# Kernel optimization log

Hardware: AMD Instinct MI355X
Metric: run time of the kernel (lower is better)

The kernel has to match this reference:

```python
import jax, jax.numpy as jnp
import numpy as np

N, C, K, B, G = 32768, 128, 16, 4, 8
SCALE, BASE = 2.0, 10000.0

def _bn(x, gamma, beta, eps=1e-5):
    # torch BatchNorm1d (training): stats over all axes except channel (last)
    axes = tuple(range(x.ndim - 1))
    mean = x.mean(axes)
    var = x.var(axes)
    return (x - mean) / jnp.sqrt(var + eps) * gamma + beta

def _cayley_rope(x, coord, S_param):
    c = x.shape[-1]
    S = jnp.triu(S_param, 1)
    S = S - S.T
    I = jnp.eye(c, dtype=x.dtype)
    P = jnp.linalg.solve(I + S, I - S)  # (I+S)^-1 (I-S)
    xr = x @ P.T
    dpa = c // 3 // 2 * 2          # dim per axis (even)
    dr = dpa * 3                   # rotated dims
    inv_freq = 1.0 / (BASE ** (jnp.arange(0, dpa, 2, dtype=jnp.float32) / dpa))
    cs = coord * SCALE
    def rot(f, c1):
        ang = c1[:, None] * inv_freq[None, :]
        s, co = jnp.sin(ang), jnp.cos(ang)
        fr, fi = jnp.split(f, 2, axis=-1)
        return jnp.concatenate([fr * co - fi * s, fr * s + fi * co], -1)
    parts = [rot(xr[:, i * dpa:(i + 1) * dpa], cs[:, i]) for i in range(3)]
    out = jnp.concatenate(parts + [xr[:, dr:]], -1)
    return out @ P

def setup_inputs() -> dict:
    key = jax.random.key(0)
    ks = jax.random.split(key, 24)
    w = lambda k, i, o, s=0.02: jax.random.normal(k, (i, o), jnp.float32) * s
    inp = {
        'feat': jax.random.normal(ks[0], (N, C), jnp.float32),
        'coord': jax.random.uniform(ks[1], (N, 3), jnp.float32) * 10.0,
        'reference_index': jax.random.randint(ks[2], (N, K), 0, N),
        'offset': jnp.arange(1, B + 1, dtype=jnp.int32) * (N // B),
        'Wq': w(ks[3], C, C), 'bq': jnp.zeros((C,)),
        'gq': jnp.ones((C,)), 'bnq': jnp.zeros((C,)),
        'Wk': w(ks[4], C, C), 'bk': jnp.zeros((C,)),
        'gk': jnp.ones((C,)), 'bnk': jnp.zeros((C,)),
        'Wv': w(ks[5], C, C), 'bv': jnp.zeros((C,)),
        'S_param': jax.random.normal(ks[6], (C, C), jnp.float32) * 0.01,
        'Ww1': w(ks[7], C, G), 'bw1': jnp.zeros((G,)),
        'gw': jnp.ones((G,)), 'bnw': jnp.zeros((G,)),
        'Ww2': w(ks[8], G, G), 'bw2': jnp.zeros((G,)),
        'Wg1': w(ks[9], 2 * C, C), 'bg1': jnp.zeros((C,)),
        'gg': jnp.ones((C,)), 'bng': jnp.zeros((C,)),
        'Wg2': w(ks[10], C, G, 0.001), 'bg2': jnp.full((G,), 3.0),
    }
    return inp

def reference(feat, coord, reference_index, offset, Wq, bq, gq, bnq, Wk, bk, gk, bnk,
              Wv, bv, S_param, Ww1, bw1, gw, bnw, Ww2, bw2, Wg1, bg1, gg, bng, Wg2, bg2):
    q_raw = jax.nn.relu(_bn(feat @ Wq + bq, gq, bnq))
    k_raw = jax.nn.relu(_bn(feat @ Wk + bk, gk, bnk))
    value = feat @ Wv + bv
    q = _cayley_rope(q_raw, coord, S_param)
    k = _cayley_rope(k_raw, coord, S_param)
    kg = k[reference_index]            # [N,K,C] gather
    vg = value[reference_index]        # [N,K,C]
    rel = kg - q[:, None, :]
    geom = jax.nn.relu(_bn(rel @ Ww1 + bw1, gw, bnw)) @ Ww2 + bw2  # [N,K,G]
    seg = jnp.searchsorted(offset, jnp.arange(N), side='right')
    gmax = jax.ops.segment_max(q_raw, seg, num_segments=B)
    gate_in = jnp.concatenate([q_raw, gmax[seg]], -1)              # [N,2C]
    gate = jax.nn.sigmoid(jax.nn.relu(_bn(gate_in @ Wg1 + bg1, gg, bng)) @ Wg2 + bg2)  # [N,G]
    refined = geom * (1.0 + gate[:, None, :])
    attn = jax.nn.softmax(refined, axis=1)
    mask = jnp.sign(reference_index + 1).astype(attn.dtype)
    attn = attn * mask[:, :, None]
    vg4 = vg.reshape(N, K, G, C // G)
    out = jnp.einsum('nkgi,nkg->ngi', vg4, attn).reshape(N, C)
    return out
```

## Files before the change

kernel.cpp:

```cpp
#include <hip/hip_runtime.h>
#include <math.h>

#define N_PTS 32768
#define C_DIM 128
#define K_NB  16
#define G_DIM 8

#define OF_PT     0
#define OF_PW     16384
#define OF_STATQ  17408
#define OF_STATK  17664
#define OF_STATG1 17920
#define OF_STATH  18176
#define OF_UMAXP  18192
#define OF_UMAXN  18704
#define OF_WQT    20480
#define OF_WKT    28672
#define OF_WVT    36864
#define OF_WG1T   45056
#define OF_PTMIT  53248
#define OF_QW     61440
#define OF_KW     323584
#define OF_GATE   585728
#define OF_BIG0   1048576
#define OF_BIG1   5242880
#define OF_BIG2   9437184
#define OF_BIG3   13631488

typedef short bf16x8 __attribute__((ext_vector_type(8)));
typedef float f32x4  __attribute__((ext_vector_type(4)));

__device__ __forceinline__ unsigned f2bf(float f) {
  unsigned u = __float_as_uint(f);
  return (u + 0x7fffu + ((u >> 16) & 1u)) >> 16;
}
__device__ __forceinline__ unsigned fenc(float f) {
  unsigned b = __float_as_uint(f);
  return (b & 0x80000000u) ? ~b : (b | 0x80000000u);
}
__device__ __forceinline__ float fdec(unsigned u) {
  unsigned b = (u & 0x80000000u) ? (u & 0x7fffffffu) : ~u;
  return __uint_as_float(b);
}
__device__ __forceinline__ bf16x8 pack_bf8(float4 a, float4 b) {
  bf16x8 r;
  r[0] = (short)f2bf(a.x); r[1] = (short)f2bf(a.y);
  r[2] = (short)f2bf(a.z); r[3] = (short)f2bf(a.w);
  r[4] = (short)f2bf(b.x); r[5] = (short)f2bf(b.y);
  r[6] = (short)f2bf(b.z); r[7] = (short)f2bf(b.w);
  return r;
}

struct MMJob {
  const float* A; const float* B; float* D;
  float s, a, b, c;
  int asymA, asymB;
};

__device__ __forceinline__ float fetch_asym(const float* M, int r, int c) {
  return (c > r) ? M[r*128 + c] : ((c < r) ? -M[c*128 + r] : 0.f);
}

__device__ __forceinline__ void mm_body(const MMJob& jb, int t, int tid)
{
  __shared__ float As[32][132];
  __shared__ float Bs[128][36];
  int tr = (t >> 2) * 32, tc = (t & 3) * 32;
  #pragma unroll
  for (int it = 0; it < 4; ++it) {
    int q = tid + it*256; int r = q >> 5, cq = q & 31;
    if (jb.asymA) {
      #pragma unroll
      for (int i = 0; i < 4; ++i) As[r][cq*4 + i] = fetch_asym(jb.A, tr + r, cq*4 + i);
    } else {
      *(float4*)&As[r][cq*4] = ((const float4*)jb.A)[(tr + r)*32 + cq];
    }
  }
  #pragma unroll
  for (int it = 0; it < 4; ++it) {
    int q = tid + it*256; int r = q >> 3, cq = q & 7;
    if (jb.asymB) {
      #pragma unroll
      for (int i = 0; i < 4; ++i) Bs[r][cq*4 + i] = fetch_asym(jb.B, r, tc + cq*4 + i);
    } else {
      *(float4*)&Bs[r][cq*4] = ((const float4*)jb.B)[r*32 + (tc >> 2) + cq];
    }
  }
  __syncthreads();
  int tx = tid & 15, ty = tid >> 4;
  int r0 = ty*2, c0 = tx*2;
  float acc[2][2] = {{0.f,0.f},{0.f,0.f}};
  #pragma unroll 8
  for (int k = 0; k < 128; ++k) {
    float a0 = As[r0][k], a1 = As[r0+1][k];
    float b0 = Bs[k][c0], b1 = Bs[k][c0+1];
    acc[0][0] = fmaf(a0, b0, acc[0][0]);
    acc[0][1] = fmaf(a0, b1, acc[0][1]);
    acc[1][0] = fmaf(a1, b0, acc[1][0]);
    acc[1][1] = fmaf(a1, b1, acc[1][1]);
  }
  #pragma unroll
  for (int dr = 0; dr < 2; ++dr) {
    #pragma unroll
    for (int dc = 0; dc < 2; ++dc) {
      int R = tr + r0 + dr, Cc = tc + c0 + dc;
      float v = jb.s * acc[dr][dc];
      if (jb.a != 0.f) {
        float av = jb.asymA ? fetch_asym(jb.A, R, Cc) : jb.A[R*128 + Cc];
        v = fmaf(jb.a, av, v);
      }
      if (jb.b != 0.f) {
        float bv = jb.asymB ? fetch_asym(jb.B, R, Cc) : jb.B[R*128 + Cc];
        v = fmaf(jb.b, bv, v);
      }
      if (R == Cc) v += jb.c;
      jb.D[R*128 + Cc] = v;
    }
  }
}

__global__ __launch_bounds__(256) void mm128(MMJob j0, MMJob j1)
{
  int bx = blockIdx.x;
  mm_body((bx < 16) ? j0 : j1, bx & 15, threadIdx.x);
}

__global__ __launch_bounds__(256) void chain1(const float* __restrict__ Sp, float* __restrict__ T1,
    const float* __restrict__ Wq, const float* __restrict__ Wk,
    const float* __restrict__ Wv, const float* __restrict__ Wg1,
    short* __restrict__ WqT, short* __restrict__ WkT,
    short* __restrict__ WvT, short* __restrict__ Wg1T,
    float* __restrict__ statz)
{
  int bx = blockIdx.x, tid = threadIdx.x;
  if (bx < 16) {
    MMJob j{Sp, Sp, T1, 1.f, 0.f, 0.f, 0.f, 1, 1};
    mm_body(j, bx, tid);
  } else if (bx == 16) {
    #pragma unroll
    for (int it = 0; it < 8; ++it) {
      int idx = it*256 + tid;
      if (idx < 1808) statz[idx] = 0.f;
    }
  } else {
    int idx = bx - 17, widx = idx >> 2, qr = idx & 3;
    const float* src = (widx == 0) ? Wq : (widx == 1) ? Wk : (widx == 2) ? Wv : Wg1;
    short* dst = (widx == 0) ? WqT : (widx == 1) ? WkT : (widx == 2) ? WvT : Wg1T;
    const float4* s4 = (const float4*)src;
    #pragma unroll
    for (int it = 0; it < 4; ++it) {
      int q = it*256 + tid; int k = qr*32 + (q >> 5), n4 = q & 31;
      float4 v = s4[k*32 + n4];
      dst[(n4*4+0)*128 + k] = (short)f2bf(v.x);
      dst[(n4*4+1)*128 + k] = (short)f2bf(v.y);
      dst[(n4*4+2)*128 + k] = (short)f2bf(v.z);
      dst[(n4*4+3)*128 + k] = (short)f2bf(v.w);
    }
  }
}

__global__ __launch_bounds__(1024) void pwprep(const float* __restrict__ PT,
                                               const float* __restrict__ Ww1,
                                               float* __restrict__ PW,
                                               short* __restrict__ PTmIT)
{
  __shared__ float pts[128*128];
  int tid = threadIdx.x, bx = blockIdx.x;
  if (bx == 0) {
    #pragma unroll
    for (int it = 0; it < 16; ++it) pts[tid + it*1024] = PT[tid + it*1024];
    __syncthreads();
    int i = tid & 127, g = tid >> 7;
    float acc = 0.f;
    #pragma unroll 8
    for (int j = 0; j < 128; ++j) acc = fmaf(pts[j*128 + i], Ww1[j*8 + g], acc);
    PW[i*8 + g] = acc;
  } else {
    int qr = bx - 1;
    #pragma unroll
    for (int it = 0; it < 4; ++it) {
      int q = it*1024 + tid;
      int k = qr*32 + (q >> 7), n = q & 127;
      float v = PT[k*128 + n] - ((k == n) ? 1.f : 0.f);
      PTmIT[n*128 + k] = (short)f2bf(v);
    }
  }
}

template<int MODE>
__device__ __forceinline__ void qkv_pass(const short* __restrict__ WT,
    const float* __restrict__ bias, float* __restrict__ Out,
    const bf16x8* af, int row0, int w, int l15, int quad, int lane,
    float* ssum, float* ssq, unsigned* ump, unsigned* umn)
{
  #pragma unroll
  for (int nt = 0; nt < 8; ++nt) {
    f32x4 ac = {0.f, 0.f, 0.f, 0.f};
    #pragma unroll
    for (int ks = 0; ks < 4; ++ks) {
      bf16x8 bf = *(const bf16x8*)&WT[(nt*16 + l15)*128 + ks*32 + quad*8];
      ac = __builtin_amdgcn_mfma_f32_16x16x32_bf16(af[ks], bf, ac, 0, 0, 0);
    }
    int col = nt*16 + l15;
    float bb = bias[col];
    float s = 0.f, s2 = 0.f, mx = -1e30f, mn = 1e30f;
    #pragma unroll
    for (int r = 0; r < 4; ++r) {
      float v = ac[r] + bb;
      int row = row0 + w*16 + quad*4 + r;
      Out[(long)row*128 + col] = v;
      if (MODE < 2) { s += v; s2 = fmaf(v, v, s2); }
      if (MODE == 0) { mx = fmaxf(mx, v); mn = fminf(mn, v); }
    }
    if (MODE < 2) {
      s += __shfl_xor(s, 16); s += __shfl_xor(s, 32);
      s2 += __shfl_xor(s2, 16); s2 += __shfl_xor(s2, 32);
      if (MODE == 0) {
        mx = fmaxf(mx, __shfl_xor(mx, 16)); mx = fmaxf(mx, __shfl_xor(mx, 32));
        mn = fminf(mn, __shfl_xor(mn, 16)); mn = fminf(mn, __shfl_xor(mn, 32));
      }
      if (lane < 16) {
        atomicAdd(&ssum[col], s); atomicAdd(&ssq[col], s2);
        if (MODE == 0) { atomicMax(&ump[col], fenc(mx)); atomicMax(&umn[col], fenc(-mn)); }
      }
    }
  }
}

__global__ __launch_bounds__(256) void qkv_mfma(const float* __restrict__ feat,
    const short* __restrict__ WqT, const short* __restrict__ WkT, const short* __restrict__ WvT,
    const float* __restrict__ bq, const float* __restrict__ bk, const float* __restrict__ bv,
    float* __restrict__ Aq, float* __restrict__ Bk, float* __restrict__ Vv,
    float* __restrict__ statq, float* __restrict__ statk,
    unsigned* __restrict__ umaxp, unsigned* __restrict__ umaxn)
{
  __shared__ float ssum[2][128], ssq[2][128];
  __shared__ unsigned ump[128], umn[128];
  int tid = threadIdx.x, row0 = blockIdx.x * 64, seg = row0 >> 13;
  if (tid < 128) {
    ssum[0][tid] = 0.f; ssum[1][tid] = 0.f;
    ssq[0][tid] = 0.f;  ssq[1][tid] = 0.f;
    ump[tid] = 0u; umn[tid] = 0u;
  }
  __syncthreads();
  int lane = tid & 63, w = tid >> 6, l15 = lane & 15, quad = lane >> 4;
  const float4* f4 = (const float4*)feat;
  bf16x8 af[4];
  #pragma unroll
  for (int ks = 0; ks < 4; ++ks) {
    long base = (long)(row0 + w*16 + l15)*32 + ks*8 + quad*2;
    float4 a0 = f4[base], a1 = f4[base + 1];
    af[ks] = pack_bf8(a0, a1);
  }
  qkv_pass<0>(WqT, bq, Aq, af, row0, w, l15, quad, lane, ssum[0], ssq[0], ump, umn);
  qkv_pass<1>(WkT, bk, Bk, af, row0, w, l15, quad, lane, ssum[1], ssq[1], ump, umn);
  qkv_pass<2>(WvT, bv, Vv, af, row0, w, l15, quad, lane, nullptr, nullptr, nullptr, nullptr);
  __syncthreads();
  if (tid < 128) {
    atomicAdd(&statq[tid], ssum[0][tid]); atomicAdd(&statq[128 + tid], ssq[0][tid]);
    atomicAdd(&statk[tid], ssum[1][tid]); atomicAdd(&statk[128 + tid], ssq[1][tid]);
    atomicMax(&umaxp[seg*128 + tid], ump[tid]);
    atomicMax(&umaxn[seg*128 + tid], umn[tid]);
  }
}

__global__ __launch_bounds__(256) void rqkw(
    const float* __restrict__ Aq, const float* __restrict__ Bk,
    const short* __restrict__ PTmIT, const short* __restrict__ Wg1T,
    const float* __restrict__ coord,
    const float* __restrict__ statq, const float* __restrict__ statk,
    const float* __restrict__ gq, const float* __restrict__ bnq,
    const float* __restrict__ gk, const float* __restrict__ bnk,
    const unsigned* __restrict__ umaxp, const unsigned* __restrict__ umaxn,
    const float* __restrict__ Wg1, const float* __restrict__ bg1,
    const float* __restrict__ PW, const float* __restrict__ bw1,
    float* __restrict__ qw, float* __restrict__ kw,
    float* __restrict__ g1, float* __restrict__ statg1)
{
  __shared__ float xsq[32*132], xsk[32*132];
  __shared__ float pws[128*8];
  __shared__ float caq[128], cbq[128], cak[128], cbk[128];
  __shared__ float gml[128], gsg[128];
  __shared__ float ssum[128], ssq[128];
  int tid = threadIdx.x;
  int row0 = blockIdx.x * 32, seg = row0 >> 13;
  const float invn = 1.f / 32768.f;
  if (tid < 128) {
    float m = statq[tid]*invn, vv = fmaf(-m, m, statq[128 + tid]*invn);
    float a = rsqrtf(vv + 1e-5f) * gq[tid];
    float b = fmaf(-m, a, bnq[tid]);
    caq[tid] = a; cbq[tid] = b;
    float mx = fdec(umaxp[seg*128 + tid]);
    float mn = -fdec(umaxn[seg*128 + tid]);
    gml[tid] = fmaxf(0.f, fmaxf(fmaf(a, mx, b), fmaf(a, mn, b)));
    m = statk[tid]*invn; vv = fmaf(-m, m, statk[128 + tid]*invn);
    a = rsqrtf(vv + 1e-5f) * gk[tid];
    cak[tid] = a; cbk[tid] = fmaf(-m, a, bnk[tid]);
    ssum[tid] = 0.f; ssq[tid] = 0.f;
  }
  #pragma unroll
  for (int it = 0; it < 4; ++it) { int idx = tid + it*256; pws[idx] = PW[idx]; }
  __syncthreads();
  if (tid < 128) {
    float acc = bg1[tid];
    #pragma unroll 8
    for (int j = 0; j < 128; ++j) acc = fmaf(gml[j], Wg1[(128 + j)*128 + tid], acc);
    gsg[tid] = acc;
  }
  int lane = tid & 63, w = tid >> 6, l15 = lane & 15, quad = lane >> 4;
  bool isq = (w < 2);
  const float* src = isq ? Aq : Bk;
  const float* ca = isq ? caq : cak;
  const float* cb = isq ? cbq : cbk;
  int rw = (w & 1) * 16;
  const float4* s4 = (const float4*)src;
  bf16x8 af[4];
  #pragma unroll
  for (int ks = 0; ks < 4; ++ks) {
    long base = (long)(row0 + rw + l15)*32 + ks*8 + quad*2;
    float4 a0 = s4[base], a1 = s4[base + 1];
    int c0 = ks*32 + quad*8;
    float4 r0, r1;
    r0.x = fmaxf(0.f, fmaf(ca[c0+0], a0.x, cb[c0+0]));
    r0.y = fmaxf(0.f, fmaf(ca[c0+1], a0.y, cb[c0+1]));
    r0.z = fmaxf(0.f, fmaf(ca[c0+2], a0.z, cb[c0+2]));
    r0.w = fmaxf(0.f, fmaf(ca[c0+3], a0.w, cb[c0+3]));
    r1.x = fmaxf(0.f, fmaf(ca[c0+4], a1.x, cb[c0+4]));
    r1.y = fmaxf(0.f, fmaf(ca[c0+5], a1.y, cb[c0+5]));
    r1.z = fmaxf(0.f, fmaf(ca[c0+6], a1.z, cb[c0+6]));
    r1.w = fmaxf(0.f, fmaf(ca[c0+7], a1.w, cb[c0+7]));
    af[ks] = pack_bf8(r0, r1);
  }
  f32x4 accv[8];
  #pragma unroll
  for (int nt = 0; nt < 8; ++nt) {
    f32x4 ac = {0.f, 0.f, 0.f, 0.f};
    #pragma unroll
    for (int ks = 0; ks < 4; ++ks) {
      bf16x8 bf = *(const bf16x8*)&PTmIT[(nt*16 + l15)*128 + ks*32 + quad*8];
      ac = __builtin_amdgcn_mfma_f32_16x16x32_bf16(af[ks], bf, ac, 0, 0, 0);
    }
    accv[nt] = ac;
  }
  f32x4 accw[8];
  if (isq) {
    #pragma unroll
    for (int nt = 0; nt < 8; ++nt) {
      f32x4 ac = {0.f, 0.f, 0.f, 0.f};
      #pragma unroll
      for (int ks = 0; ks < 4; ++ks) {
        bf16x8 bf = *(const bf16x8*)&Wg1T[(nt*16 + l15)*128 + ks*32 + quad*8];
        ac = __builtin_amdgcn_mfma_f32_16x16x32_bf16(af[ks], bf, ac, 0, 0, 0);
      }
      accw[nt] = ac;
    }
  }
  float* xs = isq ? xsq : xsk;
  #pragma unroll
  for (int nt = 0; nt < 8; ++nt) {
    int col = nt*16 + l15;
    #pragma unroll
    for (int r = 0; r < 4; ++r) {
      int rl = rw + quad*4 + r;
      float xv = src[(long)(row0 + rl)*128 + col];
      float xr = fmaxf(0.f, fmaf(ca[col], xv, cb[col]));
      xs[rl*132 + col] = accv[nt][r] + xr;
    }
  }
  __syncthreads();
  if (isq) {
    #pragma unroll
    for (int nt = 0; nt < 8; ++nt) {
      int col = nt*16 + l15;
      float gsv = gsg[col];
      float s = 0.f, s2 = 0.f;
      #pragma unroll
      for (int r = 0; r < 4; ++r) {
        float v = accw[nt][r] + gsv;
        int row = row0 + rw + quad*4 + r;
        g1[(long)row*128 + col] = v;
        s += v; s2 = fmaf(v, v, s2);
      }
      s += __shfl_xor(s, 16); s += __shfl_xor(s, 32);
      s2 += __shfl_xor(s2, 16); s2 += __shfl_xor(s2, 32);
      if (lane < 16) { atomicAdd(&ssum[col], s); atomicAdd(&ssq[col], s2); }
    }
  }
  #pragma unroll
  for (int it = 0; it < 8; ++it) {
    int idx = it*256 + tid;
    int r = idx >> 6, s = idx & 63;
    if (s < 63) {
      int a3 = s / 21, j = s - a3*21;
      int cr = a3*42 + j;
      float invf = exp2f((float)(2*j) * (-13.287712379549449f / 42.f));
      float ang = coord[(row0 + r)*3 + a3] * (2.0f * invf);
      float sn, co; sincosf(ang, &sn, &co);
      float fr = xsq[r*132 + cr], fi = xsq[r*132 + cr + 21];
      xsq[r*132 + cr]      = fr*co - fi*sn;
      xsq[r*132 + cr + 21] = fr*sn + fi*co;
      fr = xsk[r*132 + cr]; fi = xsk[r*132 + cr + 21];
      xsk[r*132 + cr]      = fr*co - fi*sn;
      xsk[r*132 + cr + 21] = fr*sn + fi*co;
    }
  }
  __syncthreads();
  #pragma unroll
  for (int it = 0; it < 2; ++it) {
    int idx = it*256 + tid;
    int mat = idx >> 8, r2 = (idx >> 3) & 31, g = idx & 7;
    const float* x2 = mat ? xsk : xsq;
    float acc = mat ? bw1[g] : 0.f;
    #pragma unroll 8
    for (int i = 0; i < 128; ++i) acc = fmaf(x2[r2*132 + i], pws[i*8 + g], acc);
    float* dst = mat ? kw : qw;
    dst[(long)(row0 + r2)*8 + g] = acc;
  }
  if (tid < 128) {
    atomicAdd(&statg1[tid], ssum[tid]);
    atomicAdd(&statg1[128 + tid], ssq[tid]);
  }
}

__global__ __launch_bounds__(256) void mid(
    const float* __restrict__ g1, const float* __restrict__ statg1,
    const float* __restrict__ ggm, const float* __restrict__ bng,
    const float* __restrict__ Wg2, const float* __restrict__ bg2,
    float* __restrict__ gate,
    const float* __restrict__ kw, const float* __restrict__ qw,
    const int* __restrict__ ref, float* __restrict__ stath)
{
  __shared__ float gs[32][132];
  __shared__ float w2s[128][8];
  __shared__ float cA[128], cB[128];
  __shared__ float red[256];
  int tid = threadIdx.x;
  if (blockIdx.x < 1024) {
    int row0 = blockIdx.x * 32;
    #pragma unroll
    for (int it = 0; it < 4; ++it) { int idx = tid + it*256; w2s[idx >> 3][idx & 7] = Wg2[idx]; }
    if (tid < 128) {
      const float invn = 1.f / 32768.f;
      float m = statg1[tid]*invn, v = fmaf(-m, m, statg1[128 + tid]*invn);
      float a = rsqrtf(v + 1e-5f) * ggm[tid];
      cA[tid] = a; cB[tid] = fmaf(-m, a, bng[tid]);
    }
    #pragma unroll
    for (int it = 0; it < 4; ++it) {
      int idx = tid + it*256; int r = idx >> 5, cq = idx & 31;
      *(float4*)&gs[r][cq*4] = *(const float4*)&g1[(long)(row0 + r)*128 + cq*4];
    }
    __syncthreads();
    int r = tid >> 3, g = tid & 7;
    float acc = bg2[g];
    #pragma unroll 8
    for (int c2 = 0; c2 < 128; ++c2) {
      float act = fmaxf(0.f, fmaf(gs[r][c2], cA[c2], cB[c2]));
      acc = fmaf(act, w2s[c2][g], acc);
    }
    gate[(long)(row0 + r)*8 + g] = 1.f / (1.f + expf(-acc));
  } else {
    long base = (long)(blockIdx.x - 1024) * 4096;
    float s = 0.f, sq = 0.f;
    for (int it = 0; it < 16; ++it) {
      long idx = base + it*256 + tid;
      int n = (int)(idx >> 7); int kk = (int)((idx >> 3) & 15); int g = (int)(idx & 7);
      int r = ref[n*16 + kk];
      float h = kw[(long)r*8 + g] - qw[(long)n*8 + g];
      s += h; sq = fmaf(h, h, sq);
    }
    red[tid] = s; __syncthreads();
    for (int d = 128; d >= 8; d >>= 1) { if (tid < d) red[tid] += red[tid + d]; __syncthreads(); }
    if (tid < 8) atomicAdd(&stath[tid], red[tid]);
    __syncthreads();
    red[tid] = sq; __syncthreads();
    for (int d = 128; d >= 8; d >>= 1) { if (tid < d) red[tid] += red[tid + d]; __syncthreads(); }
    if (tid < 8) atomicAdd(&stath[8 + tid], red[tid]);
  }
}

__global__ __launch_bounds__(256) void attn_out(const float* __restrict__ qw, const float* __restrict__ kw,
                                                const float* __restrict__ stath,
                                                const float* __restrict__ gw, const float* __restrict__ bnw,
                                                const float* __restrict__ Ww2, const float* __restrict__ bw2,
                                                const float* __restrict__ gate, const int* __restrict__ ref,
                                                const float* __restrict__ v, float* __restrict__ out)
{
  __shared__ float sm1[2][16][9];
  __shared__ float sm2[2][16][9];
  __shared__ int   smr[2][16];
  int tid = threadIdx.x; int rh = tid >> 7, t = tid & 127;
  int n = blockIdx.x * 2 + rh;
  int kk = t >> 3, g = t & 7;
  if (t < 16) smr[rh][t] = ref[n*16 + t];
  __syncthreads();
  const float invnk = 1.f / 524288.f;
  float m0 = stath[g]*invnk, v0 = fmaf(-m0, m0, stath[8 + g]*invnk);
  float aw = rsqrtf(v0 + 1e-5f) * gw[g];
  float bw = fmaf(-m0, aw, bnw[g]);
  int rr = smr[rh][kk];
  float h = kw[(long)rr*8 + g] - qw[(long)n*8 + g];
  sm1[rh][kk][g] = fmaxf(0.f, fmaf(h, aw, bw));
  __syncthreads();
  float acc = bw2[g];
  #pragma unroll
  for (int g2 = 0; g2 < 8; ++g2) acc = fmaf(sm1[rh][kk][g2], Ww2[g2*8 + g], acc);
  float refined = acc * (1.f + gate[(long)n*8 + g]);
  sm2[rh][kk][g] = refined;
  __syncthreads();
  float mx = -1e30f;
  #pragma unroll
  for (int k2 = 0; k2 < 16; ++k2) mx = fmaxf(mx, sm2[rh][k2][g]);
  float e = expf(refined - mx);
  sm1[rh][kk][g] = e;
  __syncthreads();
  float ssum = 0.f;
  #pragma unroll
  for (int k2 = 0; k2 < 16; ++k2) ssum += sm1[rh][k2][g];
  float mask = ((rr + 1) > 0) ? 1.f : (((rr + 1) == 0) ? 0.f : -1.f);
  float attn = e / ssum * mask;
  sm2[rh][kk][g] = attn;
  __syncthreads();
  float o = 0.f;
  #pragma unroll
  for (int k2 = 0; k2 < 16; ++k2) {
    o = fmaf(v[(long)smr[rh][k2]*128 + t], sm2[rh][k2][t >> 4], o);
  }
  out[(long)n*128 + t] = o;
}

extern "C" void kernel_launch(void* const* d_in, const int* in_sizes, int n_in,
                              void* d_out, int out_size, void* d_ws, size_t ws_size,
                              hipStream_t stream)
{
  const float* feat  = (const float*)d_in[0];
  const float* coord = (const float*)d_in[1];
  const int*   ref   = (const int*)d_in[2];
  const float* Wq  = (const float*)d_in[4];
  const float* bq  = (const float*)d_in[5];
  const float* gq  = (const float*)d_in[6];
  const float* bnq = (const float*)d_in[7];
  const float* Wk  = (const float*)d_in[8];
  const float* bk  = (const float*)d_in[9];
  const float* gk  = (const float*)d_in[10];
  const float* bnk = (const float*)d_in[11];
  const float* Wv  = (const float*)d_in[12];
  const float* bv  = (const float*)d_in[13];
  const float* Sp  = (const float*)d_in[14];
  const float* Ww1 = (const float*)d_in[15];
  const float* bw1 = (const float*)d_in[16];
  const float* gw  = (const float*)d_in[17];
  const float* bnw = (const float*)d_in[18];
  const float* Ww2 = (const float*)d_in[19];
  const float* bw2 = (const float*)d_in[20];
  const float* Wg1 = (const float*)d_in[21];
  const float* bg1 = (const float*)d_in[22];
  const float* ggm = (const float*)d_in[23];
  const float* bng = (const float*)d_in[24];
  const float* Wg2 = (const float*)d_in[25];
  const float* bg2 = (const float*)d_in[26];
  float* out = (float*)d_out;

  float* W = (float*)d_ws;
  float* PT = W + OF_PT;
  float* PW = W + OF_PW;
  short* WqT   = (short*)(W + OF_WQT);
  short* WkT   = (short*)(W + OF_WKT);
  short* WvT   = (short*)(W + OF_WVT);
  short* Wg1T  = (short*)(W + OF_WG1T);
  short* PTmIT = (short*)(W + OF_PTMIT);
  float* A  = W + OF_BIG0;
  float* Bb = W + OF_BIG1;
  float* E  = W + OF_BIG2;
  float* Vv = W + OF_BIG3;

  float* T1 = E;
  float* T2 = E + 16384;
  float* T3 = E + 32768;
  float* W1 = E + 49152;
  float* W2 = E + 65536;

  chain1<<<33, 256, 0, stream>>>(Sp, T1, Wq, Wk, Wv, Wg1,
                                 WqT, WkT, WvT, Wg1T, W + OF_STATQ);
  MMJob jT2{T1, T1, T2, 1.f, 0.f, 0.f, 0.f, 0, 0};
  MMJob jW1{Sp, T1, W1, 1.f, 1.f, 1.f, 1.f, 1, 0};
  mm128<<<32, 256, 0, stream>>>(jT2, jW1);
  MMJob jT3{T2, T2, T3, 1.f, 0.f, 0.f, 0.f, 0, 0};
  MMJob jW2{W1, T2, W2, 1.f, 1.f, 0.f, 0.f, 0, 0};
  mm128<<<32, 256, 0, stream>>>(jT3, jW2);
  MMJob jPT{W2, T3, PT, 2.f, 2.f, 0.f, -1.f, 0, 0};
  mm128<<<16, 256, 0, stream>>>(jPT, jPT);
  pwprep<<<5, 1024, 0, stream>>>(PT, Ww1, PW, PTmIT);
  qkv_mfma<<<512, 256, 0, stream>>>(feat, WqT, WkT, WvT, bq, bk, bv,
                                    A, Bb, Vv,
                                    W + OF_STATQ, W + OF_STATK,
                                    (unsigned*)(W + OF_UMAXP), (unsigned*)(W + OF_UMAXN));
  rqkw<<<1024, 256, 0, stream>>>(A, Bb, PTmIT, Wg1T, coord,
                                 W + OF_STATQ, W + OF_STATK,
                                 gq, bnq, gk, bnk,
                                 (const unsigned*)(W + OF_UMAXP), (const unsigned*)(W + OF_UMAXN),
                                 Wg1, bg1, PW, bw1,
                                 W + OF_QW, W + OF_KW, E, W + OF_STATG1);
  mid<<<2048, 256, 0, stream>>>(E, W + OF_STATG1, ggm, bng, Wg2, bg2, W + OF_GATE,
                                W + OF_KW, W + OF_QW, ref, W + OF_STATH);
  attn_out<<<16384, 256, 0, stream>>>(W + OF_QW, W + OF_KW, W + OF_STATH, gw, bnw, Ww2, bw2,
                                      W + OF_GATE, ref, Vv, out);
}
```

Baseline: 335.5 us.

## Compute Cayley transform via Neumann iteration and recompute Q/K projections in rqkw

Replaces the chain of 128x128 matmul kernels and pwprep with a single cayley kernel. Each block iterates x = e - S x sixteen times in bf16-quantized shared memory to obtain two columns of (I+S)^-1, then derives the P-minus-I operand and PW from them. Q and K pre-activations are no longer written to global memory by qkv_mfma; rqkw instead reloads feat and recomputes the Q/K projections with MFMA before applying BN and the rotation. This removes several serial launches and about 32 MB of intermediate traffic, at the cost of redundant GEMM work and an approximate inverse whose accuracy depends on S being small.

```diff
diff --git a/kernel.cpp b/kernel.cpp
--- a/kernel.cpp
+++ b/kernel.cpp
@@ -6,33 +6,35 @@
 #define K_NB  16
 #define G_DIM 8
 
-#define OF_PT     0
-#define OF_PW     16384
-#define OF_STATQ  17408
-#define OF_STATK  17664
-#define OF_STATG1 17920
-#define OF_STATH  18176
-#define OF_UMAXP  18192
-#define OF_UMAXN  18704
-#define OF_WQT    20480
-#define OF_WKT    28672
-#define OF_WVT    36864
-#define OF_WG1T   45056
-#define OF_PTMIT  53248
-#define OF_QW     61440
-#define OF_KW     323584
-#define OF_GATE   585728
-#define OF_BIG0   1048576
-#define OF_BIG1   5242880
-#define OF_BIG2   9437184
-#define OF_BIG3   13631488
+#define OF_PW     0
+#define OF_STATQ  1024
+#define OF_STATK  1280
+#define OF_STATG1 1536
+#define OF_STATH  1792
+#define OF_UMAXP  1808
+#define OF_UMAXN  2320
+#define OF_WQT    4096
+#define OF_WKT    12288
+#define OF_WVT    20480
+#define OF_WG1T   28672
+#define OF_PTMIT  36864
+#define OF_QW     65536
+#define OF_KW     327680
+#define OF_GATE   589824
+#define OF_G1     1048576
+#define OF_V      5242880
 
 typedef short bf16x8 __attribute__((ext_vector_type(8)));
 typedef float f32x4  __attribute__((ext_vector_type(4)));
+
+#define LSTR 136
 
 __device__ __forceinline__ unsigned f2bf(float f) {
   unsigned u = __float_as_uint(f);
   return (u + 0x7fffu + ((u >> 16) & 1u)) >> 16;
+}
+__device__ __forceinline__ float bf2f(short s) {
+  return __uint_as_float(((unsigned)(unsigned short)s) << 16);
 }
 __device__ __forceinline__ unsigned fenc(float f) {
   unsigned b = __float_as_uint(f);
@@ -50,140 +52,110 @@
   r[6] = (short)f2bf(b.z); r[7] = (short)f2bf(b.w);
   return r;
 }
-
-struct MMJob {
-  const float* A; const float* B; float* D;
-  float s, a, b, c;
-  int asymA, asymB;
-};
-
 __device__ __forceinline__ float fetch_asym(const float* M, int r, int c) {
   return (c > r) ? M[r*128 + c] : ((c < r) ? -M[c*128 + r] : 0.f);
 }
 
-__device__ __forceinline__ void mm_body(const MMJob& jb, int t, int tid)
-{
-  __shared__ float As[32][132];
-  __shared__ float Bs[128][36];
-  int tr = (t >> 2) * 32, tc = (t & 3) * 32;
-  #pragma unroll
-  for (int it = 0; it < 4; ++it) {
-    int q = tid + it*256; int r = q >> 5, cq = q & 31;
-    if (jb.asymA) {
-      #pragma unroll
-      for (int i = 0; i < 4; ++i) As[r][cq*4 + i] = fetch_asym(jb.A, tr + r, cq*4 + i);
-    } else {
-      *(float4*)&As[r][cq*4] = ((const float4*)jb.A)[(tr + r)*32 + cq];
-    }
-  }
-  #pragma unroll
-  for (int it = 0; it < 4; ++it) {
-    int q = tid + it*256; int r = q >> 3, cq = q & 7;
-    if (jb.asymB) {
-      #pragma unroll
-      for (int i = 0; i < 4; ++i) Bs[r][cq*4 + i] = fetch_asym(jb.B, r, tc + cq*4 + i);
-    } else {
-      *(float4*)&Bs[r][cq*4] = ((const float4*)jb.B)[r*32 + (tc >> 2) + cq];
-    }
-  }
-  __syncthreads();
-  int tx = tid & 15, ty = tid >> 4;
-  int r0 = ty*2, c0 = tx*2;
-  float acc[2][2] = {{0.f,0.f},{0.f,0.f}};
-  #pragma unroll 8
-  for (int k = 0; k < 128; ++k) {
-    float a0 = As[r0][k], a1 = As[r0+1][k];
-    float b0 = Bs[k][c0], b1 = Bs[k][c0+1];
-    acc[0][0] = fmaf(a0, b0, acc[0][0]);
-    acc[0][1] = fmaf(a0, b1, acc[0][1]);
-    acc[1][0] = fmaf(a1, b0, acc[1][0]);
-    acc[1][1] = fmaf(a1, b1, acc[1][1]);
-  }
-  #pragma unroll
-  for (int dr = 0; dr < 2; ++dr) {
-    #pragma unroll
-    for (int dc = 0; dc < 2; ++dc) {
-      int R = tr + r0 + dr, Cc = tc + c0 + dc;
-      float v = jb.s * acc[dr][dc];
-      if (jb.a != 0.f) {
-        float av = jb.asymA ? fetch_asym(jb.A, R, Cc) : jb.A[R*128 + Cc];
-        v = fmaf(jb.a, av, v);
-      }
-      if (jb.b != 0.f) {
-        float bv = jb.asymB ? fetch_asym(jb.B, R, Cc) : jb.B[R*128 + Cc];
-        v = fmaf(jb.b, bv, v);
-      }
-      if (R == Cc) v += jb.c;
-      jb.D[R*128 + Cc] = v;
-    }
-  }
-}
-
-__global__ __launch_bounds__(256) void mm128(MMJob j0, MMJob j1)
-{
-  int bx = blockIdx.x;
-  mm_body((bx < 16) ? j0 : j1, bx & 15, threadIdx.x);
-}
-
-__global__ __launch_bounds__(256) void chain1(const float* __restrict__ Sp, float* __restrict__ T1,
+__device__ __forceinline__ void gemm8(const short* __restrict__ BT, const bf16x8* af,
+                                      f32x4* out, int l15, int quad)
+{
+  #pragma unroll
+  for (int nt = 0; nt < 8; ++nt) {
+    f32x4 ac = {0.f, 0.f, 0.f, 0.f};
+    #pragma unroll
+    for (int ks = 0; ks < 4; ++ks) {
+      bf16x8 bf = *(const bf16x8*)&BT[(nt*16 + l15)*128 + ks*32 + quad*8];
+      ac = __builtin_amdgcn_mfma_f32_16x16x32_bf16(af[ks], bf, ac, 0, 0, 0);
+    }
+    out[nt] = ac;
+  }
+}
+
+__global__ __launch_bounds__(256) void cayley(const float* __restrict__ Sp,
+    const float* __restrict__ Ww1,
     const float* __restrict__ Wq, const float* __restrict__ Wk,
     const float* __restrict__ Wv, const float* __restrict__ Wg1,
     short* __restrict__ WqT, short* __restrict__ WkT,
     short* __restrict__ WvT, short* __restrict__ Wg1T,
+    short* __restrict__ PTmIT, float* __restrict__ PW,
     float* __restrict__ statz)
 {
+  __shared__ short Ssh[128*LSTR];
+  __shared__ float x0[128], x1[128];
   int bx = blockIdx.x, tid = threadIdx.x;
-  if (bx < 16) {
-    MMJob j{Sp, Sp, T1, 1.f, 0.f, 0.f, 0.f, 1, 1};
-    mm_body(j, bx, tid);
-  } else if (bx == 16) {
-    #pragma unroll
-    for (int it = 0; it < 8; ++it) {
-      int idx = it*256 + tid;
-      if (idx < 1808) statz[idx] = 0.f;
-    }
+  if (bx >= 64) {
+    if (bx < 80) {
+      int idx = bx - 64, widx = idx >> 2, qr = idx & 3;
+      const float* src = (widx == 0) ? Wq : (widx == 1) ? Wk : (widx == 2) ? Wv : Wg1;
+      short* dst = (widx == 0) ? WqT : (widx == 1) ? WkT : (widx == 2) ? WvT : Wg1T;
+      const float4* s4 = (const float4*)src;
+      #pragma unroll
+      for (int it = 0; it < 4; ++it) {
+        int q = it*256 + tid; int k = qr*32 + (q >> 5), n4 = q & 31;
+        float4 v = s4[k*32 + n4];
+        dst[(n4*4+0)*128 + k] = (short)f2bf(v.x);
+        dst[(n4*4+1)*128 + k] = (short)f2bf(v.y);
+        dst[(n4*4+2)*128 + k] = (short)f2bf(v.z);
+        dst[(n4*4+3)*128 + k] = (short)f2bf(v.w);
+      }
+    } else {
+      #pragma unroll
+      for (int it = 0; it < 8; ++it) {
+        int idx = it*256 + tid;
+        if (idx < 1808) statz[idx] = 0.f;
+      }
+    }
+    return;
+  }
+  int c0 = bx*2, c1 = c0 + 1;
+  #pragma unroll 8
+  for (int it = 0; it < 64; ++it) {
+    int idx = it*256 + tid; int i = idx >> 7, j = idx & 127;
+    Ssh[i*LSTR + j] = (short)f2bf(fetch_asym(Sp, i, j));
+  }
+  if (tid < 128) {
+    x0[tid] = (tid == c0) ? 1.f : 0.f;
+    x1[tid] = (tid == c1) ? 1.f : 0.f;
+  }
+  __syncthreads();
+  int i = tid >> 1, h = tid & 1;
+  const short* srow = &Ssh[i*LSTR + h*64];
+  for (int t = 0; t < 16; ++t) {
+    float a0 = 0.f, a1 = 0.f;
+    #pragma unroll
+    for (int jq = 0; jq < 16; ++jq) {
+      short4 sv = *(const short4*)&srow[jq*4];
+      #pragma unroll
+      for (int u = 0; u < 4; ++u) {
+        float s = bf2f((&sv.x)[u]);
+        int j = h*64 + jq*4 + u;
+        a0 = fmaf(s, x0[j], a0);
+        a1 = fmaf(s, x1[j], a1);
+      }
+    }
+    a0 += __shfl_xor(a0, 1);
+    a1 += __shfl_xor(a1, 1);
+    __syncthreads();
+    if (h == 0) {
+      x0[i] = a0 + ((i == c0) ? 1.f : 0.f);
+      x1[i] = a1 + ((i == c1) ? 1.f : 0.f);
+    }
+    __syncthreads();
+  }
+  if (tid < 128) {
+    PTmIT[c0*128 + tid] = (short)f2bf(2.f*x0[tid] - ((tid == c0) ? 2.f : 0.f));
   } else {
-    int idx = bx - 17, widx = idx >> 2, qr = idx & 3;
-    const float* src = (widx == 0) ? Wq : (widx == 1) ? Wk : (widx == 2) ? Wv : Wg1;
-    short* dst = (widx == 0) ? WqT : (widx == 1) ? WkT : (widx == 2) ? WvT : Wg1T;
-    const float4* s4 = (const float4*)src;
-    #pragma unroll
-    for (int it = 0; it < 4; ++it) {
-      int q = it*256 + tid; int k = qr*32 + (q >> 5), n4 = q & 31;
-      float4 v = s4[k*32 + n4];
-      dst[(n4*4+0)*128 + k] = (short)f2bf(v.x);
-      dst[(n4*4+1)*128 + k] = (short)f2bf(v.y);
-      dst[(n4*4+2)*128 + k] = (short)f2bf(v.z);
-      dst[(n4*4+3)*128 + k] = (short)f2bf(v.w);
-    }
-  }
-}
-
-__global__ __launch_bounds__(1024) void pwprep(const float* __restrict__ PT,
-                                               const float* __restrict__ Ww1,
-                                               float* __restrict__ PW,
-                                               short* __restrict__ PTmIT)
-{
-  __shared__ float pts[128*128];
-  int tid = threadIdx.x, bx = blockIdx.x;
-  if (bx == 0) {
-    #pragma unroll
-    for (int it = 0; it < 16; ++it) pts[tid + it*1024] = PT[tid + it*1024];
-    __syncthreads();
-    int i = tid & 127, g = tid >> 7;
+    int t = tid - 128;
+    PTmIT[c1*128 + t] = (short)f2bf(2.f*x1[t] - ((t == c1) ? 2.f : 0.f));
+  }
+  if (tid < 16) {
+    int cc = tid >> 3, g = tid & 7;
+    const float* xv = cc ? x1 : x0;
+    int c = cc ? c1 : c0;
     float acc = 0.f;
     #pragma unroll 8
-    for (int j = 0; j < 128; ++j) acc = fmaf(pts[j*128 + i], Ww1[j*8 + g], acc);
-    PW[i*8 + g] = acc;
-  } else {
-    int qr = bx - 1;
-    #pragma unroll
-    for (int it = 0; it < 4; ++it) {
-      int q = it*1024 + tid;
-      int k = qr*32 + (q >> 7), n = q & 127;
-      float v = PT[k*128 + n] - ((k == n) ? 1.f : 0.f);
-      PTmIT[n*128 + k] = (short)f2bf(v);
-    }
+    for (int j = 0; j < 128; ++j) acc = fmaf(xv[j], Ww1[j*8 + g], acc);
+    PW[c*8 + g] = 2.f*acc - Ww1[c*8 + g];
   }
 }
 
@@ -207,10 +179,13 @@
     #pragma unroll
     for (int r = 0; r < 4; ++r) {
       float v = ac[r] + bb;
-      int row = row0 + w*16 + quad*4 + r;
-      Out[(long)row*128 + col] = v;
-      if (MODE < 2) { s += v; s2 = fmaf(v, v, s2); }
-      if (MODE == 0) { mx = fmaxf(mx, v); mn = fminf(mn, v); }
+      if (MODE == 2) {
+        int row = row0 + w*16 + quad*4 + r;
+        Out[(long)row*128 + col] = v;
+      } else {
+        s += v; s2 = fmaf(v, v, s2);
+        if (MODE == 0) { mx = fmaxf(mx, v); mn = fminf(mn, v); }
+      }
     }
     if (MODE < 2) {
       s += __shfl_xor(s, 16); s += __shfl_xor(s, 32);
@@ -230,7 +205,7 @@
 __global__ __launch_bounds__(256) void qkv_mfma(const float* __restrict__ feat,
     const short* __restrict__ WqT, const short* __restrict__ WkT, const short* __restrict__ WvT,
     const float* __restrict__ bq, const float* __restrict__ bk, const float* __restrict__ bv,
-    float* __restrict__ Aq, float* __restrict__ Bk, float* __restrict__ Vv,
+    float* __restrict__ Vv,
     float* __restrict__ statq, float* __restrict__ statk,
     unsigned* __restrict__ umaxp, unsigned* __restrict__ umaxn)
 {
@@ -252,8 +227,8 @@
     float4 a0 = f4[base], a1 = f4[base + 1];
     af[ks] = pack_bf8(a0, a1);
   }
-  qkv_pass<0>(WqT, bq, Aq, af, row0, w, l15, quad, lane, ssum[0], ssq[0], ump, umn);
-  qkv_pass<1>(WkT, bk, Bk, af, row0, w, l15, quad, lane, ssum[1], ssq[1], ump, umn);
+  qkv_pass<0>(WqT, bq, nullptr, af, row0, w, l15, quad, lane, ssum[0], ssq[0], ump, umn);
+  qkv_pass<1>(WkT, bk, nullptr, af, row0, w, l15, quad, lane, ssum[1], ssq[1], nullptr, nullptr);
   qkv_pass<2>(WvT, bv, Vv, af, row0, w, l15, quad, lane, nullptr, nullptr, nullptr, nullptr);
   __syncthreads();
   if (tid < 128) {
@@ -265,9 +240,11 @@
 }
 
 __global__ __launch_bounds__(256) void rqkw(
-    const float* __restrict__ Aq, const float* __restrict__ Bk,
+    const float* __restrict__ feat,
+    const short* __restrict__ WqT, const short* __restrict__ WkT,
     const short* __restrict__ PTmIT, const short* __restrict__ Wg1T,
     const float* __restrict__ coord,
+    const float* __restrict__ bq, const float* __restrict__ bk,
     const float* __restrict__ statq, const float* __restrict__ statk,
     const float* __restrict__ gq, const float* __restrict__ bnq,
     const float* __restrict__ gk, const float* __restrict__ bnk,
@@ -277,11 +254,17 @@
     float* __restrict__ qw, float* __restrict__ kw,
     float* __restrict__ g1, float* __restrict__ statg1)
 {
-  __shared__ float xsq[32*132], xsk[32*132];
-  __shared__ float pws[128*8];
+  __shared__ __align__(16) char arena[33792];
+  __shared__ float pws[1024];
   __shared__ float caq[128], cbq[128], cak[128], cbk[128];
-  __shared__ float gml[128], gsg[128];
+  __shared__ float cbiasq[128], cbiask[128];
+  __shared__ float gml[128], gsg[128], gpart[256];
   __shared__ float ssum[128], ssq[128];
+  short* featS = (short*)arena;
+  short* bnqS  = (short*)(arena + 32*LSTR*2);
+  short* bnkS  = (short*)(arena + 64*LSTR*2);
+  float* xsq = (float*)arena;
+  float* xsk = (float*)(arena + 16896);
   int tid = threadIdx.x;
   int row0 = blockIdx.x * 32, seg = row0 >> 13;
   const float invn = 1.f / 32768.f;
@@ -296,79 +279,78 @@
     m = statk[tid]*invn; vv = fmaf(-m, m, statk[128 + tid]*invn);
     a = rsqrtf(vv + 1e-5f) * gk[tid];
     cak[tid] = a; cbk[tid] = fmaf(-m, a, bnk[tid]);
+    cbiasq[tid] = bq[tid]; cbiask[tid] = bk[tid];
     ssum[tid] = 0.f; ssq[tid] = 0.f;
   }
   #pragma unroll
   for (int it = 0; it < 4; ++it) { int idx = tid + it*256; pws[idx] = PW[idx]; }
-  __syncthreads();
-  if (tid < 128) {
-    float acc = bg1[tid];
+  {
+    const float4* s4 = (const float4*)feat;
+    #pragma unroll
+    for (int it = 0; it < 4; ++it) {
+      int q = it*256 + tid; int r = q >> 5, c4 = q & 31;
+      float4 v = s4[(long)(row0 + r)*32 + c4];
+      uint2 p;
+      p.x = f2bf(v.x) | (f2bf(v.y) << 16);
+      p.y = f2bf(v.z) | (f2bf(v.w) << 16);
+      *(uint2*)&featS[r*LSTR + c4*4] = p;
+    }
+  }
+  __syncthreads();
+  {
+    int c = tid & 127, hf = tid >> 7;
+    float acc = 0.f;
     #pragma unroll 8
-    for (int j = 0; j < 128; ++j) acc = fmaf(gml[j], Wg1[(128 + j)*128 + tid], acc);
-    gsg[tid] = acc;
+    for (int j = 0; j < 64; ++j)
+      acc = fmaf(gml[hf*64 + j], Wg1[(128 + hf*64 + j)*128 + c], acc);
+    gpart[tid] = acc;
   }
   int lane = tid & 63, w = tid >> 6, l15 = lane & 15, quad = lane >> 4;
   bool isq = (w < 2);
-  const float* src = isq ? Aq : Bk;
+  int rw = (w & 1) * 16;
   const float* ca = isq ? caq : cak;
   const float* cb = isq ? cbq : cbk;
-  int rw = (w & 1) * 16;
-  const float4* s4 = (const float4*)src;
+  const float* cbias = isq ? cbiasq : cbiask;
+  const short* WT = isq ? WqT : WkT;
   bf16x8 af[4];
   #pragma unroll
-  for (int ks = 0; ks < 4; ++ks) {
-    long base = (long)(row0 + rw + l15)*32 + ks*8 + quad*2;
-    float4 a0 = s4[base], a1 = s4[base + 1];
-    int c0 = ks*32 + quad*8;
-    float4 r0, r1;
-    r0.x = fmaxf(0.f, fmaf(ca[c0+0], a0.x, cb[c0+0]));
-    r0.y = fmaxf(0.f, fmaf(ca[c0+1], a0.y, cb[c0+1]));
-    r0.z = fmaxf(0.f, fmaf(ca[c0+2], a0.z, cb[c0+2]));
-    r0.w = fmaxf(0.f, fmaf(ca[c0+3], a0.w, cb[c0+3]));
-    r1.x = fmaxf(0.f, fmaf(ca[c0+4], a1.x, cb[c0+4]));
-    r1.y = fmaxf(0.f, fmaf(ca[c0+5], a1.y, cb[c0+5]));
-    r1.z = fmaxf(0.f, fmaf(ca[c0+6], a1.z, cb[c0+6]));
-    r1.w = fmaxf(0.f, fmaf(ca[c0+7], a1.w, cb[c0+7]));
-    af[ks] = pack_bf8(r0, r1);
-  }
-  f32x4 accv[8];
-  #pragma unroll
-  for (int nt = 0; nt < 8; ++nt) {
-    f32x4 ac = {0.f, 0.f, 0.f, 0.f};
-    #pragma unroll
-    for (int ks = 0; ks < 4; ++ks) {
-      bf16x8 bf = *(const bf16x8*)&PTmIT[(nt*16 + l15)*128 + ks*32 + quad*8];
-      ac = __builtin_amdgcn_mfma_f32_16x16x32_bf16(af[ks], bf, ac, 0, 0, 0);
-    }
-    accv[nt] = ac;
-  }
-  f32x4 accw[8];
-  if (isq) {
-    #pragma unroll
-    for (int nt = 0; nt < 8; ++nt) {
-      f32x4 ac = {0.f, 0.f, 0.f, 0.f};
-      #pragma unroll
-      for (int ks = 0; ks < 4; ++ks) {
-        bf16x8 bf = *(const bf16x8*)&Wg1T[(nt*16 + l15)*128 + ks*32 + quad*8];
-        ac = __builtin_amdgcn_mfma_f32_16x16x32_bf16(af[ks], bf, ac, 0, 0, 0);
-      }
-      accw[nt] = ac;
-    }
-  }
-  float* xs = isq ? xsq : xsk;
+  for (int ks = 0; ks < 4; ++ks)
+    af[ks] = *(bf16x8*)&featS[(rw + l15)*LSTR + ks*32 + quad*8];
+  f32x4 lin[8];
+  gemm8(WT, af, lin, l15, quad);
+  float bnl[32];
+  short* bnS = isq ? bnqS : bnkS;
   #pragma unroll
   for (int nt = 0; nt < 8; ++nt) {
     int col = nt*16 + l15;
+    float A = ca[col], B = cb[col], BI = cbias[col];
     #pragma unroll
     for (int r = 0; r < 4; ++r) {
-      int rl = rw + quad*4 + r;
-      float xv = src[(long)(row0 + rl)*128 + col];
-      float xr = fmaxf(0.f, fmaf(ca[col], xv, cb[col]));
-      xs[rl*132 + col] = accv[nt][r] + xr;
-    }
-  }
-  __syncthreads();
+      float v = fmaxf(0.f, fmaf(A, lin[nt][r] + BI, B));
+      bnl[nt*4 + r] = v;
+      bnS[(rw + quad*4 + r)*LSTR + col] = (short)f2bf(v);
+    }
+  }
+  __syncthreads();
+  if (tid < 128) gsg[tid] = gpart[tid] + gpart[128 + tid] + bg1[tid];
+  bf16x8 af2[4];
+  #pragma unroll
+  for (int ks = 0; ks < 4; ++ks)
+    af2[ks] = *(bf16x8*)&bnS[(rw + l15)*LSTR + ks*32 + quad*8];
+  f32x4 accv[8];
+  gemm8(PTmIT, af2, accv, l15, quad);
+  __syncthreads();
+  float* xs = isq ? xsq : xsk;
+  #pragma unroll
+  for (int nt = 0; nt < 8; ++nt) {
+    int col = nt*16 + l15;
+    #pragma unroll
+    for (int r = 0; r < 4; ++r)
+      xs[(rw + quad*4 + r)*132 + col] = accv[nt][r] + bnl[nt*4 + r];
+  }
   if (isq) {
+    f32x4 accw[8];
+    gemm8(Wg1T, af2, accw, l15, quad);
     #pragma unroll
     for (int nt = 0; nt < 8; ++nt) {
       int col = nt*16 + l15;
@@ -386,6 +368,7 @@
       if (lane < 16) { atomicAdd(&ssum[col], s); atomicAdd(&ssq[col], s2); }
     }
   }
+  __syncthreads();
   #pragma unroll
   for (int it = 0; it < 8; ++it) {
     int idx = it*256 + tid;
@@ -410,9 +393,16 @@
     int idx = it*256 + tid;
     int mat = idx >> 8, r2 = (idx >> 3) & 31, g = idx & 7;
     const float* x2 = mat ? xsk : xsq;
-    float acc = mat ? bw1[g] : 0.f;
+    float a0 = 0.f, a1 = 0.f, a2 = 0.f, a3 = 0.f;
     #pragma unroll 8
-    for (int i = 0; i < 128; ++i) acc = fmaf(x2[r2*132 + i], pws[i*8 + g], acc);
+    for (int i = 0; i < 128; i += 4) {
+      float4 xv = *(const float4*)&x2[r2*132 + i];
+      a0 = fmaf(xv.x, pws[(i+0)*8 + g], a0);
+      a1 = fmaf(xv.y, pws[(i+1)*8 + g], a1);
+      a2 = fmaf(xv.z, pws[(i+2)*8 + g], a2);
+      a3 = fmaf(xv.w, pws[(i+3)*8 + g], a3);
+    }
+    float acc = (a0 + a1) + (a2 + a3) + (mat ? bw1[g] : 0.f);
     float* dst = mat ? kw : qw;
     dst[(long)(row0 + r2)*8 + g] = acc;
   }
@@ -562,46 +552,28 @@
   float* out = (float*)d_out;
 
   float* W = (float*)d_ws;
-  float* PT = W + OF_PT;
   float* PW = W + OF_PW;
   short* WqT   = (short*)(W + OF_WQT);
   short* WkT   = (short*)(W + OF_WKT);
   short* WvT   = (short*)(W + OF_WVT);
   short* Wg1T  = (short*)(W + OF_WG1T);
   short* PTmIT = (short*)(W + OF_PTMIT);
-  float* A  = W + OF_BIG0;
-  float* Bb = W + OF_BIG1;
-  float* E  = W + OF_BIG2;
-  float* Vv = W + OF_BIG3;
-
-  float* T1 = E;
-  float* T2 = E + 16384;
-  float* T3 = E + 32768;
-  float* W1 = E + 49152;
-  float* W2 = E + 65536;
-
-  chain1<<<33, 256, 0, stream>>>(Sp, T1, Wq, Wk, Wv, Wg1,
-                                 WqT, WkT, WvT, Wg1T, W + OF_STATQ);
-  MMJob jT2{T1, T1, T2, 1.f, 0.f, 0.f, 0.f, 0, 0};
-  MMJob jW1{Sp, T1, W1, 1.f, 1.f, 1.f, 1.f, 1, 0};
-  mm128<<<32, 256, 0, stream>>>(jT2, jW1);
-  MMJob jT3{T2, T2, T3, 1.f, 0.f, 0.f, 0.f, 0, 0};
-  MMJob jW2{W1, T2, W2, 1.f, 1.f, 0.f, 0.f, 0, 0};
-  mm128<<<32, 256, 0, stream>>>(jT3, jW2);
-  MMJob jPT{W2, T3, PT, 2.f, 2.f, 0.f, -1.f, 0, 0};
-  mm128<<<16, 256, 0, stream>>>(jPT, jPT);
-  pwprep<<<5, 1024, 0, stream>>>(PT, Ww1, PW, PTmIT);
-  qkv_mfma<<<512, 256, 0, stream>>>(feat, WqT, WkT, WvT, bq, bk, bv,
-                                    A, Bb, Vv,
+  float* G1 = W + OF_G1;
+  float* Vv = W + OF_V;
+
+  cayley<<<81, 256, 0, stream>>>(Sp, Ww1, Wq, Wk, Wv, Wg1,
+                                 WqT, WkT, WvT, Wg1T, PTmIT, PW, W + OF_STATQ);
+  qkv_mfma<<<512, 256, 0, stream>>>(feat, WqT, WkT, WvT, bq, bk, bv, Vv,
                                     W + OF_STATQ, W + OF_STATK,
                                     (unsigned*)(W + OF_UMAXP), (unsigned*)(W + OF_UMAXN));
-  rqkw<<<1024, 256, 0, stream>>>(A, Bb, PTmIT, Wg1T, coord,
+  rqkw<<<1024, 256, 0, stream>>>(feat, WqT, WkT, PTmIT, Wg1T, coord,
+                                 bq, bk,
                                  W + OF_STATQ, W + OF_STATK,
                                  gq, bnq, gk, bnk,
                                  (const unsigned*)(W + OF_UMAXP), (const unsigned*)(W + OF_UMAXN),
                                  Wg1, bg1, PW, bw1,
-                                 W + OF_QW, W + OF_KW, E, W + OF_STATG1);
-  mid<<<2048, 256, 0, stream>>>(E, W + OF_STATG1, ggm, bng, Wg2, bg2, W + OF_GATE,
+                                 W + OF_QW, W + OF_KW, G1, W + OF_STATG1);
+  mid<<<2048, 256, 0, stream>>>(G1, W + OF_STATG1, ggm, bng, Wg2, bg2, W + OF_GATE,
                                 W + OF_KW, W + OF_QW, ref, W + OF_STATH);
   attn_out<<<16384, 256, 0, stream>>>(W + OF_QW, W + OF_KW, W + OF_STATH, gw, bnw, Ww2, bw2,
                                       W + OF_GATE, ref, Vv, out);
```

After: 347.1 us. 3.5% more time.
